# Kernel optimization log

Measured on AMD Instinct MI355X. Metric: run time of the kernel, lower is better.

The kernel has to match this reference:

```python
import jax, jax.numpy as jnp
import numpy as np

B, S, D = 8, 8192, 1024
FILTER_SIZE = 4


def setup_inputs() -> dict:
    key = jax.random.key(0)
    k1, k2, k3 = jax.random.split(key, 3)
    x = jax.random.normal(k1, (B, S, D), dtype=jnp.float32)
    # projection to [bias, filter_size coefficients]
    W = jax.random.normal(k2, (D, FILTER_SIZE + 1), dtype=jnp.float32) / np.sqrt(D)
    noise = jax.random.uniform(k3, (B, S, 1), dtype=jnp.float32)
    return {"x": x, "W": W, "noise": noise}


def reference(x, W, noise):
    """Sequentially-dependent gater.
    gate_logits[i] = log p(g_i=1 | g_{<i}), gate_probs[i] = p, gate_samples[i] ~ Bernoulli(p).
    Filter weights are a linear projection of x; the per-step logit is
    bias + <coeffs, last filter_size samples> (zeros before t=0).
    Returns (gate_logits, gate_probs, gate_samples), each [B, S, 1].
    """
    b, s, d = x.shape
    fsz = W.shape[1] - 1
    # precompute_filter_weights: [B, S, 1+filter_size]
    fw = jnp.einsum('bsd,df->bsf', x, W)

    def step(window, inputs):
        # window: [B, fsz] most recent samples, oldest first
        fw_t, u_t = inputs  # [B, 1+fsz], [B]
        logit = fw_t[:, 0] + jnp.sum(window * fw_t[:, 1:], axis=-1)  # [B]
        logp = jax.nn.log_sigmoid(logit)
        p = jax.nn.sigmoid(logit)
        samp = (u_t < p).astype(x.dtype)
        new_window = jnp.concatenate([window[:, 1:], samp[:, None]], axis=1)
        return new_window, (logp, p, samp)

    window0 = jnp.zeros((b, fsz), dtype=x.dtype)
    xs = (jnp.swapaxes(fw, 0, 1), jnp.swapaxes(noise[..., 0], 0, 1))  # [S, B, ...]
    _, (logps, ps, samps) = jax.lax.scan(step, window0, xs)

    to_out = lambda a: jnp.swapaxes(a, 0, 1)[..., None]  # [S,B] -> [B,S,1]
    return to_out(logps), to_out(ps), to_out(samps)
```

## Files before the change

kernel.cpp:

```cpp
#include <hip/hip_runtime.h>
#include <cstdint>
#include <cstddef>


namespace {

constexpr int kB = 8;
constexpr int kS = 8192;
constexpr int kD = 1024;
constexpr int kRows = kB * kS;
constexpr int kT = 64;
constexpr int kCPB = kS / kT;
constexpr int kChunks = kB * kCPB;
constexpr unsigned long long kIdMap = 0xFEDCBA9876543210ull;

__device__ __forceinline__ float logit_from_state(unsigned int w,
                                                  const float4& A,
                                                  const float4& Bv) {
  const float s1 = (w & 1u) ? A.y : 0.0f;
  const float s2 = (w & 2u) ? A.z : 0.0f;
  const float s3 = (w & 4u) ? A.w : 0.0f;
  const float s4 = (w & 8u) ? Bv.x : 0.0f;
  return A.x + (((s1 + s2) + s3) + s4);
}

__device__ __forceinline__ unsigned long long compose(unsigned long long a,
                                                      unsigned long long b) {
  unsigned long long r = 0;
#pragma unroll
  for (int s = 0; s < 16; ++s) {
    const unsigned int e = (unsigned int)(a >> (4 * s)) & 15u;
    r |= ((b >> (4 * e)) & 15ull) << (4 * s);
  }
  return r;
}

}

__global__ __launch_bounds__(256, 4) void proj_kernel(
    const float* __restrict__ x, const float* __restrict__ W,
    const float* __restrict__ noise, float* __restrict__ fwu) {
  __shared__ float Wl[kD * 5];
  const int tid = threadIdx.x;

  const float4* W4 = reinterpret_cast<const float4*>(W);
  float4* Wl4 = reinterpret_cast<float4*>(Wl);
#pragma unroll
  for (int i = 0; i < 5; ++i) Wl4[tid + 256 * i] = W4[tid + 256 * i];
  __syncthreads();

  const int lane = tid & 63;
  const int wid = blockIdx.x * 4 + (tid >> 6);
  const int nw = gridDim.x * 4;

  float wr[4][4][5];
#pragma unroll
  for (int j = 0; j < 4; ++j)
#pragma unroll
    for (int k = 0; k < 4; ++k) {
      const int d = j * 256 + lane * 4 + k;
#pragma unroll
      for (int f = 0; f < 5; ++f) wr[j][k][f] = Wl[d * 5 + f];
    }

  for (int row = wid; row < kRows; row += nw) {
    const float4* xr = reinterpret_cast<const float4*>(x + (size_t)row * kD);
    float acc[5] = {0.f, 0.f, 0.f, 0.f, 0.f};
#pragma unroll
    for (int j = 0; j < 4; ++j) {
      const float4 v = xr[j * 64 + lane];
      const float e[4] = {v.x, v.y, v.z, v.w};
#pragma unroll
      for (int k = 0; k < 4; ++k)
#pragma unroll
        for (int f = 0; f < 5; ++f) acc[f] += e[k] * wr[j][k][f];
    }
#pragma unroll
    for (int off = 32; off >= 1; off >>= 1)
#pragma unroll
      for (int f = 0; f < 5; ++f) acc[f] += __shfl_xor(acc[f], off);

    if (lane == 0) {
      const float u = noise[row];
      const float th = logf(u / (1.0f - u));
      float4* o = reinterpret_cast<float4*>(fwu + (size_t)row * 8);
      o[0] = make_float4(acc[0], acc[1], acc[2], acc[3]);
      o[1] = make_float4(acc[4], u, th, 0.0f);
    }
  }
}

__global__ __launch_bounds__(64) void map_kernel(
    const float* __restrict__ fwu, unsigned long long* __restrict__ trajbuf,
    unsigned long long* __restrict__ maps) {
  __shared__ unsigned int end_sh[16];
  const int lane = threadIdx.x;
  const int chunk = blockIdx.x;
  const float* base = fwu + (size_t)chunk * kT * 8;

  unsigned int cur = (unsigned int)(lane & 15);
  unsigned long long traj = 0;
#pragma unroll 8
  for (int i = 0; i < kT; ++i) {
    const float4* p = reinterpret_cast<const float4*>(base + (size_t)i * 8);
    const float4 A = p[0];
    const float4 Bv = p[1];
    const unsigned int d = (logit_from_state(cur, A, Bv) > Bv.z) ? 1u : 0u;
    traj |= (unsigned long long)d << i;
    cur = (cur >> 1) | (d << 3);
  }
  if (lane < 16) {
    trajbuf[(size_t)chunk * 16 + lane] = traj;
    end_sh[lane] = cur;
  }
  __syncthreads();
  if (lane == 0) {
    unsigned long long m = 0;
#pragma unroll
    for (int s = 0; s < 16; ++s)
      m |= (unsigned long long)(end_sh[s] & 15u) << (4 * s);
    maps[chunk] = m;
  }
}

__global__ __launch_bounds__(512) void combine_kernel(
    const unsigned long long* __restrict__ maps,
    unsigned int* __restrict__ starts) {
  const int b = threadIdx.x >> 6;
  const int L = threadIdx.x & 63;
  const unsigned long long m0 = maps[b * kCPB + 2 * L];
  const unsigned long long m1 = maps[b * kCPB + 2 * L + 1];
  unsigned long long scan = compose(m0, m1);
#pragma unroll
  for (int off = 1; off < 64; off <<= 1) {
    const unsigned long long prev = __shfl_up(scan, off);
    if (L >= off) scan = compose(prev, scan);
  }
  unsigned long long pref = __shfl_up(scan, 1);
  if (L == 0) pref = kIdMap;
  const unsigned int s0 = (unsigned int)(pref & 15ull);
  starts[b * kCPB + 2 * L] = s0;
  starts[b * kCPB + 2 * L + 1] = (unsigned int)((m0 >> (4 * s0)) & 15ull);
}

__global__ __launch_bounds__(256) void emit_kernel(
    const float* __restrict__ fwu, const unsigned int* __restrict__ starts,
    const unsigned long long* __restrict__ trajbuf, float* __restrict__ out) {
  const int lane = threadIdx.x & 63;
  const int chunk = blockIdx.x * 4 + (threadIdx.x >> 6);
  const unsigned int st = starts[chunk];
  const unsigned long long traj = trajbuf[(size_t)chunk * 16 + st];
  const int row = chunk * kT + lane;

  const float4* p = reinterpret_cast<const float4*>(fwu + (size_t)row * 8);
  const float4 A = p[0];
  const float4 Bv = p[1];

  unsigned int w;
  if (lane >= 4)
    w = (unsigned int)(traj >> (lane - 4)) & 15u;
  else
    w = ((st >> lane) | ((unsigned int)traj << (4 - lane))) & 15u;

  const float logit = logit_from_state(w, A, Bv);
  const float pr = 1.0f / (1.0f + expf(-logit));
  const float lp = fminf(logit, 0.0f) - log1pf(expf(-fabsf(logit)));
  out[row] = lp;
  out[kRows + row] = pr;
  out[2 * kRows + row] = (float)((traj >> lane) & 1ull);
}

extern "C" void kernel_launch(void* const* d_in, const int* in_sizes, int n_in,
                              void* d_out, int out_size, void* d_ws,
                              size_t ws_size, hipStream_t stream) {
  const float* x = (const float*)d_in[0];
  const float* W = (const float*)d_in[1];
  const float* noise = (const float*)d_in[2];
  float* out = (float*)d_out;

  float* fwu = (float*)d_ws;
  unsigned long long* trajbuf =
      (unsigned long long*)((char*)d_ws + (size_t)kRows * 8 * sizeof(float));
  unsigned long long* maps =
      (unsigned long long*)((char*)trajbuf +
                            (size_t)kChunks * 16 * sizeof(unsigned long long));
  unsigned int* starts =
      (unsigned int*)((char*)maps + (size_t)kChunks * sizeof(unsigned long long));

  proj_kernel<<<1024, 256, 0, stream>>>(x, W, noise, fwu);
  map_kernel<<<kChunks, 64, 0, stream>>>(fwu, trajbuf, maps);
  combine_kernel<<<1, 512, 0, stream>>>(maps, starts);
  emit_kernel<<<kChunks / 4, 256, 0, stream>>>(fwu, starts, trajbuf, out);
}
```

Measured before the change: 63.38 us.

## Fuse projection with chunk map computation and combine scan with emit

The projection kernel now gives each block one 64-row chunk and keeps its results in LDS. Wave 0 then runs the 16-state chunk trajectory directly from LDS and builds the map with ballots. The separate combine kernel is folded into the emit kernel: each block redoes the per-batch 64-lane compose scan and keeps the start states in LDS. This drops two launches and a global round trip for fwu and starts, at the cost of a serial 64-step tail inside each projection block and scan work repeated in every emit block.

```diff
diff --git a/kernel.cpp b/kernel.cpp
--- a/kernel.cpp
+++ b/kernel.cpp
@@ -37,10 +37,13 @@
 
 }
 
-__global__ __launch_bounds__(256, 4) void proj_kernel(
+__global__ __launch_bounds__(256, 4) void proj_map_kernel(
     const float* __restrict__ x, const float* __restrict__ W,
-    const float* __restrict__ noise, float* __restrict__ fwu) {
+    const float* __restrict__ noise, float* __restrict__ fwu,
+    unsigned long long* __restrict__ trajbuf,
+    unsigned long long* __restrict__ maps) {
   __shared__ float Wl[kD * 5];
+  __shared__ float fl[kT * 8];
   const int tid = threadIdx.x;
 
   const float4* W4 = reinterpret_cast<const float4*>(W);
@@ -50,8 +53,9 @@
   __syncthreads();
 
   const int lane = tid & 63;
-  const int wid = blockIdx.x * 4 + (tid >> 6);
-  const int nw = gridDim.x * 4;
+  const int wv = tid >> 6;
+  const int chunk = blockIdx.x;
+  const int r0 = chunk * kT;
 
   float wr[4][4][5];
 #pragma unroll
@@ -63,7 +67,10 @@
       for (int f = 0; f < 5; ++f) wr[j][k][f] = Wl[d * 5 + f];
     }
 
-  for (int row = wid; row < kRows; row += nw) {
+#pragma unroll 1
+  for (int t = 0; t < 16; ++t) {
+    const int rl = wv * 16 + t;
+    const int row = r0 + rl;
     const float4* xr = reinterpret_cast<const float4*>(x + (size_t)row * kD);
     float acc[5] = {0.f, 0.f, 0.f, 0.f, 0.f};
 #pragma unroll
@@ -83,72 +90,79 @@
     if (lane == 0) {
       const float u = noise[row];
       const float th = logf(u / (1.0f - u));
-      float4* o = reinterpret_cast<float4*>(fwu + (size_t)row * 8);
-      o[0] = make_float4(acc[0], acc[1], acc[2], acc[3]);
-      o[1] = make_float4(acc[4], u, th, 0.0f);
-    }
-  }
-}
-
-__global__ __launch_bounds__(64) void map_kernel(
-    const float* __restrict__ fwu, unsigned long long* __restrict__ trajbuf,
-    unsigned long long* __restrict__ maps) {
-  __shared__ unsigned int end_sh[16];
-  const int lane = threadIdx.x;
-  const int chunk = blockIdx.x;
-  const float* base = fwu + (size_t)chunk * kT * 8;
-
-  unsigned int cur = (unsigned int)(lane & 15);
-  unsigned long long traj = 0;
+      const float4 o0 = make_float4(acc[0], acc[1], acc[2], acc[3]);
+      const float4 o1 = make_float4(acc[4], u, th, 0.0f);
+      float4* og = reinterpret_cast<float4*>(fwu + (size_t)row * 8);
+      og[0] = o0;
+      og[1] = o1;
+      float4* ol = reinterpret_cast<float4*>(&fl[rl * 8]);
+      ol[0] = o0;
+      ol[1] = o1;
+    }
+  }
+  __syncthreads();
+
+  if (wv == 0) {
+    unsigned int cur = (unsigned int)(lane & 15);
+    unsigned long long traj = 0;
 #pragma unroll 8
-  for (int i = 0; i < kT; ++i) {
-    const float4* p = reinterpret_cast<const float4*>(base + (size_t)i * 8);
-    const float4 A = p[0];
-    const float4 Bv = p[1];
-    const unsigned int d = (logit_from_state(cur, A, Bv) > Bv.z) ? 1u : 0u;
-    traj |= (unsigned long long)d << i;
-    cur = (cur >> 1) | (d << 3);
-  }
-  if (lane < 16) {
-    trajbuf[(size_t)chunk * 16 + lane] = traj;
-    end_sh[lane] = cur;
+    for (int i = 0; i < kT; ++i) {
+      const float4* p = reinterpret_cast<const float4*>(&fl[i * 8]);
+      const float4 A = p[0];
+      const float4 Bv = p[1];
+      const unsigned int d = (logit_from_state(cur, A, Bv) > Bv.z) ? 1u : 0u;
+      traj |= (unsigned long long)d << i;
+      cur = (cur >> 1) | (d << 3);
+    }
+    if (lane < 16) trajbuf[(size_t)chunk * 16 + lane] = traj;
+    const unsigned long long b0 = __ballot((int)(cur & 1u));
+    const unsigned long long b1 = __ballot((int)(cur & 2u));
+    const unsigned long long b2 = __ballot((int)(cur & 4u));
+    const unsigned long long b3 = __ballot((int)(cur & 8u));
+    if (lane == 0) {
+      unsigned long long m = 0;
+#pragma unroll
+      for (int s = 0; s < 16; ++s) {
+        const unsigned long long e =
+            ((b0 >> s) & 1ull) | (((b1 >> s) & 1ull) << 1) |
+            (((b2 >> s) & 1ull) << 2) | (((b3 >> s) & 1ull) << 3);
+        m |= e << (4 * s);
+      }
+      maps[chunk] = m;
+    }
+  }
+}
+
+__global__ __launch_bounds__(256) void scan_emit_kernel(
+    const float* __restrict__ fwu, const unsigned long long* __restrict__ maps,
+    const unsigned long long* __restrict__ trajbuf, float* __restrict__ out) {
+  __shared__ unsigned int starts_lds[kCPB];
+  const int tid = threadIdx.x;
+  const int lane = tid & 63;
+  const int wv = tid >> 6;
+  const int c0 = blockIdx.x * 4;
+  const int b = c0 / kCPB;
+
+  if (wv == 0) {
+    const int L = lane;
+    const unsigned long long m0 = maps[b * kCPB + 2 * L];
+    const unsigned long long m1 = maps[b * kCPB + 2 * L + 1];
+    unsigned long long scan = compose(m0, m1);
+#pragma unroll
+    for (int off = 1; off < 64; off <<= 1) {
+      const unsigned long long prev = __shfl_up(scan, off);
+      if (L >= off) scan = compose(prev, scan);
+    }
+    unsigned long long pref = __shfl_up(scan, 1);
+    if (L == 0) pref = kIdMap;
+    const unsigned int s0 = (unsigned int)(pref & 15ull);
+    starts_lds[2 * L] = s0;
+    starts_lds[2 * L + 1] = (unsigned int)((m0 >> (4 * s0)) & 15ull);
   }
   __syncthreads();
-  if (lane == 0) {
-    unsigned long long m = 0;
-#pragma unroll
-    for (int s = 0; s < 16; ++s)
-      m |= (unsigned long long)(end_sh[s] & 15u) << (4 * s);
-    maps[chunk] = m;
-  }
-}
-
-__global__ __launch_bounds__(512) void combine_kernel(
-    const unsigned long long* __restrict__ maps,
-    unsigned int* __restrict__ starts) {
-  const int b = threadIdx.x >> 6;
-  const int L = threadIdx.x & 63;
-  const unsigned long long m0 = maps[b * kCPB + 2 * L];
-  const unsigned long long m1 = maps[b * kCPB + 2 * L + 1];
-  unsigned long long scan = compose(m0, m1);
-#pragma unroll
-  for (int off = 1; off < 64; off <<= 1) {
-    const unsigned long long prev = __shfl_up(scan, off);
-    if (L >= off) scan = compose(prev, scan);
-  }
-  unsigned long long pref = __shfl_up(scan, 1);
-  if (L == 0) pref = kIdMap;
-  const unsigned int s0 = (unsigned int)(pref & 15ull);
-  starts[b * kCPB + 2 * L] = s0;
-  starts[b * kCPB + 2 * L + 1] = (unsigned int)((m0 >> (4 * s0)) & 15ull);
-}
-
-__global__ __launch_bounds__(256) void emit_kernel(
-    const float* __restrict__ fwu, const unsigned int* __restrict__ starts,
-    const unsigned long long* __restrict__ trajbuf, float* __restrict__ out) {
-  const int lane = threadIdx.x & 63;
-  const int chunk = blockIdx.x * 4 + (threadIdx.x >> 6);
-  const unsigned int st = starts[chunk];
+
+  const int chunk = c0 + wv;
+  const unsigned int st = starts_lds[chunk & (kCPB - 1)];
   const unsigned long long traj = trajbuf[(size_t)chunk * 16 + st];
   const int row = chunk * kT + lane;
 
@@ -184,11 +198,7 @@
   unsigned long long* maps =
       (unsigned long long*)((char*)trajbuf +
                             (size_t)kChunks * 16 * sizeof(unsigned long long));
-  unsigned int* starts =
-      (unsigned int*)((char*)maps + (size_t)kChunks * sizeof(unsigned long long));
-
-  proj_kernel<<<1024, 256, 0, stream>>>(x, W, noise, fwu);
-  map_kernel<<<kChunks, 64, 0, stream>>>(fwu, trajbuf, maps);
-  combine_kernel<<<1, 512, 0, stream>>>(maps, starts);
-  emit_kernel<<<kChunks / 4, 256, 0, stream>>>(fwu, starts, trajbuf, out);
-}
+
+  proj_map_kernel<<<kChunks, 256, 0, stream>>>(x, W, noise, fwu, trajbuf, maps);
+  scan_emit_kernel<<<kChunks / 4, 256, 0, stream>>>(fwu, maps, trajbuf, out);
+}
```

Result: faster. 60.35 us (-4.8%).
